# Performance work log

Hardware: AMD Instinct MI355X
Metric: run time of the kernel (lower is better)

Reference implementation:

```python
import jax, jax.numpy as jnp
import numpy as np

N_NODES = 50000
N_EDGES = 800000
IN_CH = 256
OUT_CH = 128
HID = 2 * OUT_CH  # 256
LN_EPS = 1e-5


def _add_self_loops(edge_index, n):
    loop = jnp.arange(n, dtype=edge_index.dtype)
    src = jnp.concatenate([edge_index[0], loop])
    dst = jnp.concatenate([edge_index[1], loop])
    return src, dst


def _gcn_norm(src, dst, n):
    # PyG GCNConv norm: deg over source index, symmetric normalization
    ones = jnp.ones(src.shape[0], dtype=jnp.float32)
    deg = jax.ops.segment_sum(ones, src, num_segments=n)
    dinv = jnp.where(deg > 0, deg ** -0.5, 0.0)
    return dinv[src] * dinv[dst]  # [E+N]


def _gcn_conv(x, src, dst, norm, w, b, gamma=None, beta=None):
    h = x @ w                              # [N, out]
    msgs = norm[:, None] * h[src]          # gather + scale, [E+N, out]
    out = jax.ops.segment_sum(msgs, dst, num_segments=x.shape[0])
    if gamma is not None:
        out = gamma * out + beta           # FiLM modulation (per-feature)
    return out + b


def _layernorm(x):
    mu = jnp.mean(x, axis=-1, keepdims=True)
    var = jnp.var(x, axis=-1, keepdims=True)
    return (x - mu) * jax.lax.rsqrt(var + LN_EPS)


def setup_inputs() -> dict:
    key = jax.random.key(0)
    ks = jax.random.split(key, 20)

    def g(k, shape, scale=0.05):
        return jax.random.normal(k, shape, dtype=jnp.float32) * scale

    x = jax.random.normal(ks[0], (N_NODES, IN_CH), dtype=jnp.float32)
    edge_index = jax.random.randint(ks[1], (2, N_EDGES), 0, N_NODES, dtype=jnp.int64)
    return {
        "x": x,
        "edge_index": edge_index,
        "conv1_w": g(ks[2], (IN_CH, HID)),
        "conv1_b": g(ks[3], (HID,)),
        "conv2_w": g(ks[4], (HID, OUT_CH)),
        "conv2_b": g(ks[5], (OUT_CH,)),
        "sig_conv_w": g(ks[6], (IN_CH, HID)),
        "sig_conv_b": g(ks[7], (HID,)),
        "fc1_w": g(ks[8], (HID, HID)),
        "fc1_b": g(ks[9], (HID,)),
        "fc2_w": g(ks[10], (HID, HID)),
        "fc2_b": g(ks[11], (HID,)),
        "fc3_w": g(ks[12], (OUT_CH, HID)),
        "fc3_b": g(ks[13], (OUT_CH,)),
        "fc4_w": g(ks[14], (OUT_CH, HID)),
        "fc4_b": g(ks[15], (OUT_CH,)),
    }


def reference(x, edge_index, conv1_w, conv1_b, conv2_w, conv2_b,
              sig_conv_w, sig_conv_b, fc1_w, fc1_b, fc2_w, fc2_b,
              fc3_w, fc3_b, fc4_w, fc4_b):
    n = x.shape[0]
    src, dst = _add_self_loops(edge_index, n)
    norm = _gcn_norm(src, dst, n)

    # --- GraphSignature (use_gcn_sig=True) ---
    s = jax.nn.relu(_gcn_conv(x, src, dst, norm, sig_conv_w, sig_conv_b))
    s = s.sum(0)  # [HID]
    gamma1 = jnp.tanh(s @ fc1_w.T + fc1_b)  # [HID]
    beta1 = jnp.tanh(s @ fc2_w.T + fc2_b)   # [HID]
    gamma2 = jnp.tanh(s @ fc3_w.T + fc3_b)  # [OUT]
    beta2 = jnp.tanh(s @ fc4_w.T + fc4_b)   # [OUT]

    # inner_loop=True: signature outputs are detached
    gamma1, beta1, gamma2, beta2 = map(jax.lax.stop_gradient,
                                       (gamma1, beta1, gamma2, beta2))

    # --- Encoder (GAE) ---
    h = jax.nn.relu(_gcn_conv(x, src, dst, norm, conv1_w, conv1_b,
                              gamma=gamma1, beta=beta1))
    h = _layernorm(h)
    out = _gcn_conv(h, src, dst, norm, conv2_w, conv2_b,
                    gamma=gamma2, beta=beta2)
    out = _layernorm(out)
    return out
```

## Files before the change

kernel.cpp:

```cpp
#include <hip/hip_runtime.h>

typedef _Float16 f16;
typedef f16 f16x8 __attribute__((ext_vector_type(8)));
typedef float f32x4 __attribute__((ext_vector_type(4)));
typedef unsigned short u16;
typedef unsigned int u32;

#define IN_CH  256
#define HID    256
#define OUT_CH 128
#define LN_EPS 1e-5f
#define NSLOT  32
#define NR     4
#define NC     64
#define RS     12544
#define HT     512


__global__ __launch_bounds__(HT) void k_hist(const int* __restrict__ ei, int nE, int nN,
                                             int* __restrict__ hP) {
    __shared__ int h[RS];
    int r = blockIdx.x & (NR - 1), c = blockIdx.x >> 2;
    int rsz = (nN + NR - 1) / NR;
    int r0 = r * rsz;
    int sz = nN - r0; if (sz > rsz) sz = rsz;
    for (int i = threadIdx.x; i < sz; i += HT) h[i] = 0;
    __syncthreads();
    int nT = nE + nN;
    int chunk = (nT + NC - 1) / NC;
    int e0 = c * chunk, e1 = e0 + chunk; if (e1 > nT) e1 = nT;
    for (int eb = e0 + (int)threadIdx.x; eb < e1; eb += HT * 4) {
        int ss[4], dd[4];
        #pragma unroll
        for (int u = 0; u < 4; u++) {
            int e = eb + u * HT;
            ss[u] = -1; dd[u] = -1;
            if (e < e1) {
                if (e < nE) { ss[u] = ei[e]; dd[u] = ei[nE + e]; }
                else { ss[u] = e - nE; dd[u] = e - nE; }
            }
        }
        #pragma unroll
        for (int u = 0; u < 4; u++) {
            if ((unsigned)(ss[u] - r0) < (unsigned)sz) atomicAdd(&h[ss[u] - r0], 1);
            if ((unsigned)(dd[u] - r0) < (unsigned)sz) atomicAdd(&h[dd[u] - r0], 0x10000);
        }
    }
    __syncthreads();
    for (int i = threadIdx.x; i < sz; i += HT) hP[(size_t)c * nN + r0 + i] = h[i];
}


__global__ __launch_bounds__(256) void k_alloc(const int* __restrict__ hP,
                                               int* __restrict__ rowstart,
                                               int* __restrict__ chunkbase,
                                               int* __restrict__ cnt_tot,
                                               float* __restrict__ dinv,
                                               int* __restrict__ ctr, int nN,
                                               const float* __restrict__ x, f16* __restrict__ xh,
                                               int nelem, int nAllocB, int nCast,
                                               const float* __restrict__ sigw,
                                               const float* __restrict__ c1w,
                                               const float* __restrict__ c2w,
                                               f16* __restrict__ Wt1, f16* __restrict__ Wt2) {
    int bid = blockIdx.x;
    if (bid < nAllocB) {
        int i = bid * 256 + threadIdx.x;
        int lane = threadIdx.x & 63;
        int cnt = 0, dg = 0;
        if (i < nN) {
            for (int c = 0; c < NC; c++) {
                unsigned pk = (unsigned)hP[(size_t)c * nN + i];
                cnt += (int)(pk >> 16);
                dg  += (int)(pk & 0xffffu);
            }
        }
        int p = cnt;
        #pragma unroll
        for (int off = 1; off < 64; off <<= 1) {
            int v = __shfl_up(p, off, 64);
            if (lane >= off) p += v;
        }
        int tot = __shfl(p, 63, 64);
        int base = 0;
        if (lane == 0) base = atomicAdd(ctr, tot);
        base = __shfl(base, 0, 64);
        if (i < nN) {
            int nb = base + p - cnt;
            rowstart[i] = nb;
            cnt_tot[i] = cnt;
            dinv[i] = rsqrtf((float)dg);
            int run = nb;
            for (int c = 0; c < NC; c++) {
                chunkbase[(size_t)c * nN + i] = run;
                run += (int)((unsigned)hP[(size_t)c * nN + i] >> 16);
            }
        }
    } else if (bid < nAllocB + nCast) {
        int i = (bid - nAllocB) * 2048 + threadIdx.x * 8;
        if (i >= nelem) return;
        float4 a = *(const float4*)(x + i);
        float4 b = *(const float4*)(x + i + 4);
        f16x8 o = { (f16)a.x, (f16)a.y, (f16)a.z, (f16)a.w,
                    (f16)b.x, (f16)b.y, (f16)b.z, (f16)b.w };
        *(f16x8*)(xh + i) = o;
    } else {
        int i = (bid - nAllocB - nCast) * 256 + threadIdx.x;
        if (i < 16384) {
            int ct = i >> 9;
            int rem = i & 511;
            int kx = rem >> 6;
            int lane = rem & 63;
            int q = lane >> 4, l = lane & 15;
            int n = (ct & 15) * 16 + l;
            int k0 = kx * 32 + q * 8;
            const float* src = (ct < 16) ? sigw : c1w;
            f16x8 o;
            #pragma unroll
            for (int j = 0; j < 8; j++) o[j] = (f16)src[(size_t)(k0 + j) * 256 + n];
            *(f16x8*)(Wt1 + (size_t)i * 8) = o;
        } else {
            int h = i - 16384;
            int ct = h >> 9;
            int rem = h & 511;
            int kx = rem >> 6;
            int lane = rem & 63;
            int q = lane >> 4, l = lane & 15;
            int n = ct * 16 + l;
            int k0 = kx * 32 + q * 8;
            f16x8 o;
            #pragma unroll
            for (int j = 0; j < 8; j++) o[j] = (f16)c2w[(size_t)(k0 + j) * 128 + n];
            *(f16x8*)(Wt2 + (size_t)h * 8) = o;
        }
    }
}


__global__ __launch_bounds__(HT) void k_fill(const int* __restrict__ ei, int nE, int nN,
                                             const int* __restrict__ chunkbase,
                                             u16* __restrict__ src_sorted) {
    __shared__ int pos_[RS];
    int r = blockIdx.x & (NR - 1), c = blockIdx.x >> 2;
    int rsz = (nN + NR - 1) / NR;
    int r0 = r * rsz;
    int sz = nN - r0; if (sz > rsz) sz = rsz;
    for (int i = threadIdx.x; i < sz; i += HT)
        pos_[i] = chunkbase[(size_t)c * nN + r0 + i];
    __syncthreads();
    int nT = nE + nN;
    int chunk = (nT + NC - 1) / NC;
    int e0 = c * chunk, e1 = e0 + chunk; if (e1 > nT) e1 = nT;
    for (int eb = e0 + (int)threadIdx.x; eb < e1; eb += HT * 4) {
        int ss[4], dd[4];
        #pragma unroll
        for (int u = 0; u < 4; u++) {
            int e = eb + u * HT;
            ss[u] = -1; dd[u] = -1;
            if (e < e1) {
                if (e < nE) { ss[u] = ei[e]; dd[u] = ei[nE + e]; }
                else { ss[u] = e - nE; dd[u] = e - nE; }
            }
        }
        #pragma unroll
        for (int u = 0; u < 4; u++) {
            int l = dd[u] - r0;
            if ((unsigned)l < (unsigned)sz) {
                int pos = atomicAdd(&pos_[l], 1);
                src_sorted[pos] = (u16)ss[u];
            }
        }
    }
}


__global__ __launch_bounds__(256) void k_aggX(const f16* __restrict__ xh,
                                              const int* __restrict__ rowstart,
                                              const int* __restrict__ counts,
                                              const u16* __restrict__ srcs,
                                              const float* __restrict__ dinv,
                                              f16* __restrict__ AX, int nN) {
    int wv = threadIdx.x >> 6;
    int lane = threadIdx.x & 63;
    int node = blockIdx.x * 4 + wv;
    if (node >= nN) return;
    int h = lane >> 5, sub = lane & 31;
    int beg = rowstart[node];
    int cnt = counts[node];
    float acc0[8] = {}, acc1[8] = {};
    for (int base = 0; base < cnt; base += 64) {
        int el = base + lane;
        int sv = 0; float dv = 0.f;
        if (el < cnt) { sv = srcs[beg + el]; dv = dinv[sv]; }
        int rem = cnt - base; if (rem > 64) rem = 64;
        int e = 0;
        for (; e + 16 <= rem; e += 16) {
            int s_[8]; float n_[8];
            #pragma unroll
            for (int u = 0; u < 8; u++) {
                int ii = e + u * 2 + h;
                s_[u] = __shfl(sv, ii, 64);
                n_[u] = __shfl(dv, ii, 64);
            }
            f16x8 v_[8];
            #pragma unroll
            for (int u = 0; u < 8; u++)
                v_[u] = *(const f16x8*)(xh + (size_t)s_[u] * 256 + sub * 8);
            #pragma unroll
            for (int u = 0; u < 8; u++)
                #pragma unroll
                for (int j = 0; j < 8; j++) {
                    float* a = (u & 1) ? acc1 : acc0;
                    a[j] = fmaf(n_[u], (float)v_[u][j], a[j]);
                }
        }
        for (; e < rem; e += 8) {
            int i0 = e + h, i1 = e + 2 + h, i2 = e + 4 + h, i3 = e + 6 + h;
            int sa = __shfl(sv, i0, 64), sb = __shfl(sv, i1, 64);
            int sc = __shfl(sv, i2, 64), sd = __shfl(sv, i3, 64);
            float na = __shfl(dv, i0, 64), nb = __shfl(dv, i1, 64);
            float nc = __shfl(dv, i2, 64), nd = __shfl(dv, i3, 64);
            if (i0 >= rem) na = 0.f;
            if (i1 >= rem) nb = 0.f;
            if (i2 >= rem) nc = 0.f;
            if (i3 >= rem) nd = 0.f;
            f16x8 va = *(const f16x8*)(xh + (size_t)sa * 256 + sub * 8);
            f16x8 vb = *(const f16x8*)(xh + (size_t)sb * 256 + sub * 8);
            f16x8 vc = *(const f16x8*)(xh + (size_t)sc * 256 + sub * 8);
            f16x8 vd = *(const f16x8*)(xh + (size_t)sd * 256 + sub * 8);
            #pragma unroll
            for (int j = 0; j < 8; j++) {
                acc0[j] = fmaf(na, (float)va[j], acc0[j]);
                acc1[j] = fmaf(nb, (float)vb[j], acc1[j]);
                acc0[j] = fmaf(nc, (float)vc[j], acc0[j]);
                acc1[j] = fmaf(nd, (float)vd[j], acc1[j]);
            }
        }
    }
    float dn = dinv[node];
    #pragma unroll
    for (int j = 0; j < 8; j++) {
        acc0[j] += acc1[j];
        acc0[j] += __shfl_xor(acc0[j], 32, 64);
    }
    if (lane < 32) {
        f16x8 o;
        #pragma unroll
        for (int j = 0; j < 8; j++) o[j] = (f16)(acc0[j] * dn);
        *(f16x8*)(AX + (size_t)node * 256 + sub * 8) = o;
    }
}


__global__ __launch_bounds__(256) void k_gemm_sig(const f16* __restrict__ AX,
                                                  const f16* __restrict__ Wt,
                                                  const float* __restrict__ sigb,
                                                  float* __restrict__ sig_part, int M) {
    __shared__ f16 tile[32][264];
    int t = threadIdx.x;
    int w = t >> 6, lane = t & 63, quad = lane >> 4, l16 = lane & 15;
    int m0 = blockIdx.x * 32;
    int cb = w * 64;
    f32x4 acc[2][4] = {};
    for (int kx = 0; kx < 8; kx++) {
        int ka = kx * 32 + quad * 8;
        f16x8 a[2];
        #pragma unroll
        for (int ms = 0; ms < 2; ms++) {
            int row = m0 + ms * 16 + l16; if (row >= M) row = M - 1;
            a[ms] = *(const f16x8*)(AX + (size_t)row * 256 + ka);
        }
        #pragma unroll
        for (int ns = 0; ns < 4; ns++) {
            int ct = w * 4 + ns;
            f16x8 b = *(const f16x8*)(Wt + ((size_t)((ct * 8 + kx) * 64 + lane) << 3));
            acc[0][ns] = __builtin_amdgcn_mfma_f32_16x16x32_f16(a[0], b, acc[0][ns], 0, 0, 0);
            acc[1][ns] = __builtin_amdgcn_mfma_f32_16x16x32_f16(a[1], b, acc[1][ns], 0, 0, 0);
        }
    }
    #pragma unroll
    for (int ms = 0; ms < 2; ms++)
        #pragma unroll
        for (int ns = 0; ns < 4; ns++)
            #pragma unroll
            for (int r = 0; r < 4; r++) {
                int mr = ms * 16 + quad * 4 + r;
                int c = cb + ns * 16 + l16;
                float v = fmaxf(acc[ms][ns][r] + sigb[c], 0.f);
                if (m0 + mr >= M) v = 0.f;
                tile[mr][c] = (f16)v;
            }
    __syncthreads();
    float s = 0.f;
    #pragma unroll 8
    for (int r = 0; r < 32; r++) s += (float)tile[r][t];
    atomicAdd(&sig_part[(blockIdx.x & (NSLOT - 1)) * 256 + t], s);
}


__global__ __launch_bounds__(256) void k_fc(const float* __restrict__ sig_part,
                                            const float* __restrict__ f1w, const float* __restrict__ f1b,
                                            const float* __restrict__ f2w, const float* __restrict__ f2b,
                                            const float* __restrict__ f3w, const float* __restrict__ f3b,
                                            const float* __restrict__ f4w, const float* __restrict__ f4b,
                                            const float* __restrict__ c1b, const float* __restrict__ c2b,
                                            float* __restrict__ g1, float* __restrict__ bc1,
                                            float* __restrict__ g2, float* __restrict__ bc2) {
    __shared__ float ss[256];
    int t = threadIdx.x;
    float s = 0.f;
    for (int k = 0; k < NSLOT; k++) s += sig_part[k * 256 + t];
    ss[t] = s;
    __syncthreads();
    int wv = t >> 6, lane = t & 63;
    float s0 = ss[lane], s1 = ss[lane + 64], s2v = ss[lane + 128], s3 = ss[lane + 192];
    #pragma unroll
    for (int rr = 0; rr < 16; rr++) {
        int row = blockIdx.x * 64 + wv * 16 + rr;
        const float* w; const float* bb; const float* ex; float* dst; int r;
        if (row < 256)      { w = f1w; bb = f1b; dst = g1;  ex = 0;   r = row; }
        else if (row < 512) { w = f2w; bb = f2b; dst = bc1; ex = c1b; r = row - 256; }
        else if (row < 640) { w = f3w; bb = f3b; dst = g2;  ex = 0;   r = row - 512; }
        else                { w = f4w; bb = f4b; dst = bc2; ex = c2b; r = row - 640; }
        const float* wr = w + (size_t)r * 256;
        float a = wr[lane] * s0;
        a = fmaf(wr[lane + 64], s1, a);
        a = fmaf(wr[lane + 128], s2v, a);
        a = fmaf(wr[lane + 192], s3, a);
        #pragma unroll
        for (int off = 1; off < 64; off <<= 1) a += __shfl_xor(a, off, 64);
        if (lane == 0) dst[r] = tanhf(a + bb[r]) + (ex ? ex[r] : 0.f);
    }
}


__global__ __launch_bounds__(256) void k_c1f(const f16* __restrict__ AX,
                                             const f16* __restrict__ Wt,
                                             const f16* __restrict__ Wt2,
                                             const float* __restrict__ g1,
                                             const float* __restrict__ bc1,
                                             const float* __restrict__ dinv,
                                             f16* __restrict__ HW, int M) {
    __shared__ f16 ht[32][264];
    __shared__ float ps[32][5], ps2[32][5];
    __shared__ float mu_[32], rr_[32], sdinv[32];
    int t = threadIdx.x;
    int w = t >> 6, lane = t & 63, quad = lane >> 4, l16 = lane & 15;
    int m0 = blockIdx.x * 32;
    int cb = w * 64;
    f32x4 acc[2][4] = {};
    for (int kx = 0; kx < 8; kx++) {
        int ka = kx * 32 + quad * 8;
        f16x8 a[2];
        #pragma unroll
        for (int ms = 0; ms < 2; ms++) {
            int row = m0 + ms * 16 + l16; if (row >= M) row = M - 1;
            a[ms] = *(const f16x8*)(AX + (size_t)row * 256 + ka);
        }
        #pragma unroll
        for (int ns = 0; ns < 4; ns++) {
            int ct = w * 4 + ns;
            f16x8 b = *(const f16x8*)(Wt + ((size_t)((ct * 8 + kx) * 64 + lane) << 3));
            acc[0][ns] = __builtin_amdgcn_mfma_f32_16x16x32_f16(a[0], b, acc[0][ns], 0, 0, 0);
            acc[1][ns] = __builtin_amdgcn_mfma_f32_16x16x32_f16(a[1], b, acc[1][ns], 0, 0, 0);
        }
    }

    float rs[2][4] = {{0.f,0.f,0.f,0.f},{0.f,0.f,0.f,0.f}};
    float rs2[2][4] = {{0.f,0.f,0.f,0.f},{0.f,0.f,0.f,0.f}};
    #pragma unroll
    for (int ns = 0; ns < 4; ns++) {
        int c = cb + ns * 16 + l16;
        float gv = g1[c], bv = bc1[c];
        #pragma unroll
        for (int ms = 0; ms < 2; ms++)
            #pragma unroll
            for (int r = 0; r < 4; r++) {
                float v = fmaxf(fmaf(gv, acc[ms][ns][r], bv), 0.f);
                acc[ms][ns][r] = v;
                rs[ms][r] += v;
                rs2[ms][r] = fmaf(v, v, rs2[ms][r]);
            }
    }
    #pragma unroll
    for (int off = 1; off < 16; off <<= 1)
        #pragma unroll
        for (int ms = 0; ms < 2; ms++)
            #pragma unroll
            for (int r = 0; r < 4; r++) {
                rs[ms][r]  += __shfl_xor(rs[ms][r], off, 64);
                rs2[ms][r] += __shfl_xor(rs2[ms][r], off, 64);
            }
    if (l16 == 0) {
        #pragma unroll
        for (int ms = 0; ms < 2; ms++)
            #pragma unroll
            for (int r = 0; r < 4; r++) {
                int mr = ms * 16 + quad * 4 + r;
                ps[mr][w] = rs[ms][r];
                ps2[mr][w] = rs2[ms][r];
            }
    }
    __syncthreads();
    if (t < 32) {
        float S = ps[t][0] + ps[t][1] + ps[t][2] + ps[t][3];
        float S2 = ps2[t][0] + ps2[t][1] + ps2[t][2] + ps2[t][3];
        float mu = S * (1.f / 256.f);
        mu_[t] = mu;
        rr_[t] = rsqrtf(S2 * (1.f / 256.f) - mu * mu + LN_EPS);
        int m = m0 + t;
        sdinv[t] = (m < M) ? dinv[m] : 0.f;
    }
    __syncthreads();
    #pragma unroll
    for (int ms = 0; ms < 2; ms++)
        #pragma unroll
        for (int r = 0; r < 4; r++) {
            int mr = ms * 16 + quad * 4 + r;
            float mu = mu_[mr], rr = rr_[mr];
            #pragma unroll
            for (int ns = 0; ns < 4; ns++)
                ht[mr][cb + ns * 16 + l16] = (f16)((acc[ms][ns][r] - mu) * rr);
        }
    __syncthreads();
    int cb2 = w * 32;
    f32x4 acc2[2][2] = {};
    for (int kx = 0; kx < 8; kx++) {
        int ka = kx * 32 + quad * 8;
        f16x8 a[2];
        #pragma unroll
        for (int ms = 0; ms < 2; ms++)
            a[ms] = *(const f16x8*)(&ht[ms * 16 + l16][ka]);
        #pragma unroll
        for (int ns = 0; ns < 2; ns++) {
            int ct = w * 2 + ns;
            f16x8 b = *(const f16x8*)(Wt2 + ((size_t)((ct * 8 + kx) * 64 + lane) << 3));
            acc2[0][ns] = __builtin_amdgcn_mfma_f32_16x16x32_f16(a[0], b, acc2[0][ns], 0, 0, 0);
            acc2[1][ns] = __builtin_amdgcn_mfma_f32_16x16x32_f16(a[1], b, acc2[1][ns], 0, 0, 0);
        }
    }
    #pragma unroll
    for (int ms = 0; ms < 2; ms++)
        #pragma unroll
        for (int ns = 0; ns < 2; ns++)
            #pragma unroll
            for (int r = 0; r < 4; r++) {
                int mr = ms * 16 + quad * 4 + r;
                int m = m0 + mr;
                if (m < M) HW[(size_t)m * 128 + cb2 + ns * 16 + l16] = (f16)(acc2[ms][ns][r] * sdinv[mr]);
            }
}


__global__ __launch_bounds__(256) void k_agg2(const f16* __restrict__ HW,
                                              const int* __restrict__ rowstart,
                                              const int* __restrict__ counts,
                                              const u16* __restrict__ srcs,
                                              const float* __restrict__ dinv,
                                              const float* __restrict__ g2,
                                              const float* __restrict__ bc2,
                                              float* __restrict__ out, int nN) {
    int wv = threadIdx.x >> 6;
    int lane = threadIdx.x & 63;
    int node = blockIdx.x * 4 + wv;
    if (node >= nN) return;
    int q = lane >> 4, sub = lane & 15;
    int beg = rowstart[node];
    int cnt = counts[node];
    float acc0[8] = {}, acc1[8] = {};
    for (int base = 0; base < cnt; base += 64) {
        int el = base + lane;
        int sv = 0; float dv = 0.f;
        if (el < cnt) { sv = srcs[beg + el]; dv = 1.f; }
        int rem = cnt - base; if (rem > 64) rem = 64;
        int e = 0;
        for (; e + 16 <= rem; e += 16) {
            int s_[4]; float n_[4];
            #pragma unroll
            for (int u = 0; u < 4; u++) {
                int ii = e + u * 4 + q;
                s_[u] = __shfl(sv, ii, 64);
                n_[u] = __shfl(dv, ii, 64);
            }
            f16x8 v_[4];
            #pragma unroll
            for (int u = 0; u < 4; u++)
                v_[u] = *(const f16x8*)(HW + (size_t)s_[u] * 128 + sub * 8);
            #pragma unroll
            for (int u = 0; u < 4; u++)
                #pragma unroll
                for (int j = 0; j < 8; j++) {
                    float* a = (u & 1) ? acc1 : acc0;
                    a[j] = fmaf(n_[u], (float)v_[u][j], a[j]);
                }
        }
        for (; e < rem; e += 8) {
            int i0 = e + q, i1 = e + 4 + q;
            int sa = __shfl(sv, i0, 64), sb = __shfl(sv, i1, 64);
            float na = __shfl(dv, i0, 64), nb = __shfl(dv, i1, 64);
            if (i0 >= rem) na = 0.f;
            if (i1 >= rem) nb = 0.f;
            f16x8 va = *(const f16x8*)(HW + (size_t)sa * 128 + sub * 8);
            f16x8 vb = *(const f16x8*)(HW + (size_t)sb * 128 + sub * 8);
            #pragma unroll
            for (int j = 0; j < 8; j++) {
                acc0[j] = fmaf(na, (float)va[j], acc0[j]);
                acc1[j] = fmaf(nb, (float)vb[j], acc1[j]);
            }
        }
    }
    float dn = dinv[node];
    #pragma unroll
    for (int j = 0; j < 8; j++) {
        acc0[j] += acc1[j];
        acc0[j] += __shfl_xor(acc0[j], 16, 64);
        acc0[j] += __shfl_xor(acc0[j], 32, 64);
    }
    int ch = sub * 8;
    float vfin[8];
    float s = 0.f, s2 = 0.f;
    #pragma unroll
    for (int j = 0; j < 8; j++) {
        float v = fmaf(g2[ch + j], acc0[j] * dn, bc2[ch + j]);
        vfin[j] = v;
        s += v; s2 = fmaf(v, v, s2);
    }
    #pragma unroll
    for (int off = 1; off < 16; off <<= 1) {
        s += __shfl_xor(s, off, 64);
        s2 += __shfl_xor(s2, off, 64);
    }
    float mu = s * (1.f / 128.f);
    float rr = rsqrtf(s2 * (1.f / 128.f) - mu * mu + LN_EPS);
    if (q == 0) {
        float4 o0 = { (vfin[0] - mu) * rr, (vfin[1] - mu) * rr,
                      (vfin[2] - mu) * rr, (vfin[3] - mu) * rr };
        float4 o1 = { (vfin[4] - mu) * rr, (vfin[5] - mu) * rr,
                      (vfin[6] - mu) * rr, (vfin[7] - mu) * rr };
        float* dst = out + (size_t)node * 128 + ch;
        *(float4*)dst = o0;
        *(float4*)(dst + 4) = o1;
    }
}


extern "C" void kernel_launch(void* const* d_in, const int* in_sizes, int n_in,
                              void* d_out, int out_size, void* d_ws, size_t ws_size,
                              hipStream_t stream) {
    const float* x    = (const float*)d_in[0];
    const int*   ei   = (const int*)d_in[1];
    const float* c1w  = (const float*)d_in[2];
    const float* c1b  = (const float*)d_in[3];
    const float* c2w  = (const float*)d_in[4];
    const float* c2b  = (const float*)d_in[5];
    const float* sigw = (const float*)d_in[6];
    const float* sigb = (const float*)d_in[7];
    const float* f1w  = (const float*)d_in[8];
    const float* f1b  = (const float*)d_in[9];
    const float* f2w  = (const float*)d_in[10];
    const float* f2b  = (const float*)d_in[11];
    const float* f3w  = (const float*)d_in[12];
    const float* f3b  = (const float*)d_in[13];
    const float* f4w  = (const float*)d_in[14];
    const float* f4b  = (const float*)d_in[15];
    float* out = (float*)d_out;

    int nN = in_sizes[0] / IN_CH;
    int nE = in_sizes[1] / 2;
    int nT = nE + nN;

    char* base = (char*)d_ws;
    size_t off = 0;
    auto alloc = [&](size_t bytes) { size_t o = off; off += (bytes + 255) & ~(size_t)255; return o; };

    size_t o_spart  = alloc((size_t)NSLOT * 256 * 4);
    size_t o_ctr    = alloc(256);
    size_t zero_bytes = off;
    size_t o_hP     = alloc((size_t)NC * nN * 4);
    size_t o_cbase  = alloc((size_t)NC * nN * 4);
    size_t o_g1     = alloc(256 * 4);
    size_t o_b1     = alloc(256 * 4);
    size_t o_g2     = alloc(128 * 4);
    size_t o_b2     = alloc(128 * 4);
    size_t o_rowst  = alloc((size_t)nN * 4);
    size_t o_cntt   = alloc((size_t)nN * 4);
    size_t o_dinv   = alloc((size_t)nN * 4);
    size_t o_src    = alloc((size_t)nT * 2);
    size_t o_wt1    = alloc(512 * 256 * 2);
    size_t o_wt2    = alloc(128 * 256 * 2);
    size_t o_xh     = alloc((size_t)nN * 256 * 2);
    size_t o_AX     = alloc((size_t)nN * 256 * 2);
    size_t o_HW     = alloc((size_t)nN * 128 * 2);

    float* spart  = (float*)(base + o_spart);
    int*   ctr    = (int*)(base + o_ctr);
    int*   hP     = (int*)(base + o_hP);
    int*   cbase  = (int*)(base + o_cbase);
    float* g1     = (float*)(base + o_g1);
    float* bc1    = (float*)(base + o_b1);
    float* g2     = (float*)(base + o_g2);
    float* bc2    = (float*)(base + o_b2);
    int*   rowst  = (int*)(base + o_rowst);
    int*   cntt   = (int*)(base + o_cntt);
    float* dinv   = (float*)(base + o_dinv);
    u16*   srcs   = (u16*)(base + o_src);
    f16*   Wt1    = (f16*)(base + o_wt1);
    f16*   Wt2    = (f16*)(base + o_wt2);
    f16*   xh     = (f16*)(base + o_xh);
    f16*   AX     = (f16*)(base + o_AX);
    f16*   HW     = (f16*)(base + o_HW);

    hipMemsetAsync(base, 0, zero_bytes, stream);

    k_hist<<<NR * NC, HT, 0, stream>>>(ei, nE, nN, hP);

    int nAllocB = (nN + 255) / 256;
    int nCast = (nN * IN_CH + 2047) / 2048;
    int nPrep = (512 * 256 + 128 * 256) / 2048;
    k_alloc<<<nAllocB + nCast + nPrep, 256, 0, stream>>>(hP, rowst, cbase, cntt, dinv, ctr, nN,
                                                         x, xh, nN * IN_CH, nAllocB, nCast,
                                                         sigw, c1w, c2w, Wt1, Wt2);

    k_fill<<<NR * NC, HT, 0, stream>>>(ei, nE, nN, cbase, srcs);

    int nb4 = (nN + 3) / 4;
    int mg = (nN + 31) / 32;
    k_aggX<<<nb4, 256, 0, stream>>>(xh, rowst, cntt, srcs, dinv, AX, nN);
    k_gemm_sig<<<mg, 256, 0, stream>>>(AX, Wt1, sigb, spart, nN);
    k_fc<<<12, 256, 0, stream>>>(spart, f1w, f1b, f2w, f2b, f3w, f3b, f4w, f4b,
                                 c1b, c2b, g1, bc1, g2, bc2);
    k_c1f<<<mg, 256, 0, stream>>>(AX, Wt1 + 256 * 256, Wt2, g1, bc1, dinv, HW, nN);
    k_agg2<<<nb4, 256, 0, stream>>>(HW, rowst, cntt, srcs, dinv, g2, bc2, out, nN);
}
```

Measured before the change: 331.9 us.

## Replace LDS-partitioned histogram CSR build with global-atomic degree count and fill

The CSR construction is rebuilt. Before, per-chunk shared-memory histograms were written to a large NC×nN partial array, then reduced and prefix-scanned. Now one packed degree/count word per node is accumulated with global atomics, folded into the cast/weight-prep kernel, and followed by a small scan kernel and a fill kernel that also uses global atomics. This removes the 64×nN partial-histogram reads and writes and one extra pass, but adds heavy global atomic contention, and the order of sources within each row becomes nondeterministic.

```diff
diff --git a/kernel.cpp b/kernel.cpp
--- a/kernel.cpp
+++ b/kernel.cpp
@@ -11,93 +11,34 @@
 #define OUT_CH 128
 #define LN_EPS 1e-5f
 #define NSLOT  32
-#define NR     4
-#define NC     64
-#define RS     12544
-#define HT     512
-
-
-__global__ __launch_bounds__(HT) void k_hist(const int* __restrict__ ei, int nE, int nN,
-                                             int* __restrict__ hP) {
-    __shared__ int h[RS];
-    int r = blockIdx.x & (NR - 1), c = blockIdx.x >> 2;
-    int rsz = (nN + NR - 1) / NR;
-    int r0 = r * rsz;
-    int sz = nN - r0; if (sz > rsz) sz = rsz;
-    for (int i = threadIdx.x; i < sz; i += HT) h[i] = 0;
-    __syncthreads();
+
+
+__global__ __launch_bounds__(256) void k_pre(const int* __restrict__ ei, int nE, int nN,
+                                             u32* __restrict__ pk,
+                                             const float* __restrict__ x, f16* __restrict__ xh,
+                                             int nelem, int nDeg, int nCast,
+                                             const float* __restrict__ sigw,
+                                             const float* __restrict__ c1w,
+                                             const float* __restrict__ c2w,
+                                             f16* __restrict__ Wt1, f16* __restrict__ Wt2) {
+    int bid = blockIdx.x;
     int nT = nE + nN;
-    int chunk = (nT + NC - 1) / NC;
-    int e0 = c * chunk, e1 = e0 + chunk; if (e1 > nT) e1 = nT;
-    for (int eb = e0 + (int)threadIdx.x; eb < e1; eb += HT * 4) {
-        int ss[4], dd[4];
-        #pragma unroll
-        for (int u = 0; u < 4; u++) {
-            int e = eb + u * HT;
-            ss[u] = -1; dd[u] = -1;
-            if (e < e1) {
-                if (e < nE) { ss[u] = ei[e]; dd[u] = ei[nE + e]; }
-                else { ss[u] = e - nE; dd[u] = e - nE; }
-            }
-        }
-        #pragma unroll
-        for (int u = 0; u < 4; u++) {
-            if ((unsigned)(ss[u] - r0) < (unsigned)sz) atomicAdd(&h[ss[u] - r0], 1);
-            if ((unsigned)(dd[u] - r0) < (unsigned)sz) atomicAdd(&h[dd[u] - r0], 0x10000);
-        }
-    }
-    __syncthreads();
-    for (int i = threadIdx.x; i < sz; i += HT) hP[(size_t)c * nN + r0 + i] = h[i];
-}
-
-
-__global__ __launch_bounds__(256) void k_alloc(const int* __restrict__ hP,
-                                               int* __restrict__ rowstart,
-                                               int* __restrict__ chunkbase,
-                                               int* __restrict__ cnt_tot,
-                                               float* __restrict__ dinv,
-                                               int* __restrict__ ctr, int nN,
-                                               const float* __restrict__ x, f16* __restrict__ xh,
-                                               int nelem, int nAllocB, int nCast,
-                                               const float* __restrict__ sigw,
-                                               const float* __restrict__ c1w,
-                                               const float* __restrict__ c2w,
-                                               f16* __restrict__ Wt1, f16* __restrict__ Wt2) {
-    int bid = blockIdx.x;
-    if (bid < nAllocB) {
-        int i = bid * 256 + threadIdx.x;
-        int lane = threadIdx.x & 63;
-        int cnt = 0, dg = 0;
-        if (i < nN) {
-            for (int c = 0; c < NC; c++) {
-                unsigned pk = (unsigned)hP[(size_t)c * nN + i];
-                cnt += (int)(pk >> 16);
-                dg  += (int)(pk & 0xffffu);
-            }
-        }
-        int p = cnt;
-        #pragma unroll
-        for (int off = 1; off < 64; off <<= 1) {
-            int v = __shfl_up(p, off, 64);
-            if (lane >= off) p += v;
-        }
-        int tot = __shfl(p, 63, 64);
-        int base = 0;
-        if (lane == 0) base = atomicAdd(ctr, tot);
-        base = __shfl(base, 0, 64);
-        if (i < nN) {
-            int nb = base + p - cnt;
-            rowstart[i] = nb;
-            cnt_tot[i] = cnt;
-            dinv[i] = rsqrtf((float)dg);
-            int run = nb;
-            for (int c = 0; c < NC; c++) {
-                chunkbase[(size_t)c * nN + i] = run;
-                run += (int)((unsigned)hP[(size_t)c * nN + i] >> 16);
-            }
-        }
-    } else if (bid < nAllocB + nCast) {
-        int i = (bid - nAllocB) * 2048 + threadIdx.x * 8;
+    if (bid < nDeg) {
+        int e0 = bid * 2048 + threadIdx.x;
+        #pragma unroll
+        for (int u = 0; u < 8; u++) {
+            int e = e0 + u * 256;
+            if (e < nT) {
+                if (e < nE) {
+                    atomicAdd(&pk[ei[e]], 1u);
+                    atomicAdd(&pk[ei[nE + e]], 0x10000u);
+                } else {
+                    atomicAdd(&pk[e - nE], 0x10001u);
+                }
+            }
+        }
+    } else if (bid < nDeg + nCast) {
+        int i = (bid - nDeg) * 2048 + threadIdx.x * 8;
         if (i >= nelem) return;
         float4 a = *(const float4*)(x + i);
         float4 b = *(const float4*)(x + i + 4);
@@ -105,7 +46,7 @@
                     (f16)b.x, (f16)b.y, (f16)b.z, (f16)b.w };
         *(f16x8*)(xh + i) = o;
     } else {
-        int i = (bid - nAllocB - nCast) * 256 + threadIdx.x;
+        int i = (bid - nDeg - nCast) * 256 + threadIdx.x;
         if (i < 16384) {
             int ct = i >> 9;
             int rem = i & 511;
@@ -137,38 +78,53 @@
 }
 
 
-__global__ __launch_bounds__(HT) void k_fill(const int* __restrict__ ei, int nE, int nN,
-                                             const int* __restrict__ chunkbase,
-                                             u16* __restrict__ src_sorted) {
-    __shared__ int pos_[RS];
-    int r = blockIdx.x & (NR - 1), c = blockIdx.x >> 2;
-    int rsz = (nN + NR - 1) / NR;
-    int r0 = r * rsz;
-    int sz = nN - r0; if (sz > rsz) sz = rsz;
-    for (int i = threadIdx.x; i < sz; i += HT)
-        pos_[i] = chunkbase[(size_t)c * nN + r0 + i];
-    __syncthreads();
+__global__ __launch_bounds__(256) void k_scan(const u32* __restrict__ pk,
+                                              int* __restrict__ rowstart,
+                                              int* __restrict__ wpos,
+                                              int* __restrict__ cnt_tot,
+                                              float* __restrict__ dinv,
+                                              int* __restrict__ ctr, int nN) {
+    int i = blockIdx.x * 256 + threadIdx.x;
+    int lane = threadIdx.x & 63;
+    int cnt = 0, dg = 0;
+    if (i < nN) {
+        u32 p = pk[i];
+        cnt = (int)(p >> 16);
+        dg  = (int)(p & 0xffffu);
+    }
+    int p = cnt;
+    #pragma unroll
+    for (int off = 1; off < 64; off <<= 1) {
+        int v = __shfl_up(p, off, 64);
+        if (lane >= off) p += v;
+    }
+    int tot = __shfl(p, 63, 64);
+    int base = 0;
+    if (lane == 0) base = atomicAdd(ctr, tot);
+    base = __shfl(base, 0, 64);
+    if (i < nN) {
+        int nb = base + p - cnt;
+        rowstart[i] = nb;
+        wpos[i] = nb;
+        cnt_tot[i] = cnt;
+        dinv[i] = rsqrtf((float)dg);
+    }
+}
+
+
+__global__ __launch_bounds__(256) void k_fill(const int* __restrict__ ei, int nE, int nN,
+                                              int* __restrict__ wpos,
+                                              u16* __restrict__ src_sorted) {
     int nT = nE + nN;
-    int chunk = (nT + NC - 1) / NC;
-    int e0 = c * chunk, e1 = e0 + chunk; if (e1 > nT) e1 = nT;
-    for (int eb = e0 + (int)threadIdx.x; eb < e1; eb += HT * 4) {
-        int ss[4], dd[4];
-        #pragma unroll
-        for (int u = 0; u < 4; u++) {
-            int e = eb + u * HT;
-            ss[u] = -1; dd[u] = -1;
-            if (e < e1) {
-                if (e < nE) { ss[u] = ei[e]; dd[u] = ei[nE + e]; }
-                else { ss[u] = e - nE; dd[u] = e - nE; }
-            }
-        }
-        #pragma unroll
-        for (int u = 0; u < 4; u++) {
-            int l = dd[u] - r0;
-            if ((unsigned)l < (unsigned)sz) {
-                int pos = atomicAdd(&pos_[l], 1);
-                src_sorted[pos] = (u16)ss[u];
-            }
+    int e0 = blockIdx.x * 2048 + threadIdx.x;
+    #pragma unroll
+    for (int u = 0; u < 8; u++) {
+        int e = e0 + u * 256;
+        if (e < nT) {
+            int s, d;
+            if (e < nE) { s = ei[e]; d = ei[nE + e]; } else { s = d = e - nE; }
+            int pos = atomicAdd(&wpos[d], 1);
+            src_sorted[pos] = (u16)s;
         }
     }
 }
@@ -575,14 +531,14 @@
 
     size_t o_spart  = alloc((size_t)NSLOT * 256 * 4);
     size_t o_ctr    = alloc(256);
+    size_t o_pk     = alloc((size_t)nN * 4);
     size_t zero_bytes = off;
-    size_t o_hP     = alloc((size_t)NC * nN * 4);
-    size_t o_cbase  = alloc((size_t)NC * nN * 4);
     size_t o_g1     = alloc(256 * 4);
     size_t o_b1     = alloc(256 * 4);
     size_t o_g2     = alloc(128 * 4);
     size_t o_b2     = alloc(128 * 4);
     size_t o_rowst  = alloc((size_t)nN * 4);
+    size_t o_wpos   = alloc((size_t)nN * 4);
     size_t o_cntt   = alloc((size_t)nN * 4);
     size_t o_dinv   = alloc((size_t)nN * 4);
     size_t o_src    = alloc((size_t)nT * 2);
@@ -594,13 +550,13 @@
 
     float* spart  = (float*)(base + o_spart);
     int*   ctr    = (int*)(base + o_ctr);
-    int*   hP     = (int*)(base + o_hP);
-    int*   cbase  = (int*)(base + o_cbase);
+    u32*   pk     = (u32*)(base + o_pk);
     float* g1     = (float*)(base + o_g1);
     float* bc1    = (float*)(base + o_b1);
     float* g2     = (float*)(base + o_g2);
     float* bc2    = (float*)(base + o_b2);
     int*   rowst  = (int*)(base + o_rowst);
+    int*   wpos   = (int*)(base + o_wpos);
     int*   cntt   = (int*)(base + o_cntt);
     float* dinv   = (float*)(base + o_dinv);
     u16*   srcs   = (u16*)(base + o_src);
@@ -612,16 +568,15 @@
 
     hipMemsetAsync(base, 0, zero_bytes, stream);
 
-    k_hist<<<NR * NC, HT, 0, stream>>>(ei, nE, nN, hP);
-
-    int nAllocB = (nN + 255) / 256;
+    int nDeg  = (nT + 2047) / 2048;
     int nCast = (nN * IN_CH + 2047) / 2048;
     int nPrep = (512 * 256 + 128 * 256) / 2048;
-    k_alloc<<<nAllocB + nCast + nPrep, 256, 0, stream>>>(hP, rowst, cbase, cntt, dinv, ctr, nN,
-                                                         x, xh, nN * IN_CH, nAllocB, nCast,
-                                                         sigw, c1w, c2w, Wt1, Wt2);
-
-    k_fill<<<NR * NC, HT, 0, stream>>>(ei, nE, nN, cbase, srcs);
+    k_pre<<<nDeg + nCast + nPrep, 256, 0, stream>>>(ei, nE, nN, pk, x, xh, nN * IN_CH,
+                                                    nDeg, nCast, sigw, c1w, c2w, Wt1, Wt2);
+
+    k_scan<<<(nN + 255) / 256, 256, 0, stream>>>(pk, rowst, wpos, cntt, dinv, ctr, nN);
+
+    k_fill<<<nDeg, 256, 0, stream>>>(ei, nE, nN, wpos, srcs);
 
     int nb4 = (nN + 3) / 4;
     int mg = (nN + 31) / 32;
```

New measurement: 404.7 us. +21.9%, slower.
